# Kernel optimization log

Hardware: AMD Instinct MI355X
Metric: run time of the kernel (lower is better)

Reference implementation:

```python
import jax, jax.numpy as jnp
import numpy as np
from jax import lax

NB_DIGITS = 2
BASE = 10
NUMS = BASE ** NB_DIGITS            # 100 possible values per number
SUMS = 2 * (NUMS - 1) + 1           # 199 possible sums (circuit roots)
B = 4096                            # logical batch size
N_IMAGES = B * 2 * NB_DIGITS        # 16384 digit images


def setup_inputs() -> dict:
    key = jax.random.key(0)
    ks = jax.random.split(key, 11)
    s = 0.1
    return {
        "images": jax.random.normal(ks[0], (N_IMAGES, 1, 28, 28), jnp.float32),
        "conv1_w": jax.random.normal(ks[1], (6, 1, 5, 5), jnp.float32) * s,
        "conv1_b": jax.random.normal(ks[2], (6,), jnp.float32) * s,
        "conv2_w": jax.random.normal(ks[3], (16, 6, 5, 5), jnp.float32) * s,
        "conv2_b": jax.random.normal(ks[4], (16,), jnp.float32) * s,
        "fc1_w": jax.random.normal(ks[5], (120, 256), jnp.float32) * s,
        "fc1_b": jax.random.normal(ks[6], (120,), jnp.float32) * s,
        "fc2_w": jax.random.normal(ks[7], (84, 120), jnp.float32) * s,
        "fc2_b": jax.random.normal(ks[8], (84,), jnp.float32) * s,
        "fc3_w": jax.random.normal(ks[9], (10, 84), jnp.float32) * s,
        "fc3_b": jax.random.normal(ks[10], (10,), jnp.float32) * s,
    }


def _conv(x, w, b):
    y = lax.conv_general_dilated(x, w, (1, 1), 'VALID',
                                 dimension_numbers=('NCHW', 'OIHW', 'NCHW'))
    return y + b[None, :, None, None]


def _maxpool2(x):
    return lax.reduce_window(x, -jnp.inf, lax.max, (1, 1, 2, 2), (1, 1, 2, 2), 'VALID')


def _lenet(x, c1w, c1b, c2w, c2b, f1w, f1b, f2w, f2b, f3w, f3b):
    x = jax.nn.relu(_maxpool2(_conv(x, c1w, c1b)))   # [N,6,12,12]
    x = jax.nn.relu(_maxpool2(_conv(x, c2w, c2b)))   # [N,16,4,4]
    x = x.reshape(-1, 16 * 4 * 4)
    x = jax.nn.relu(x @ f1w.T + f1b)
    x = jax.nn.relu(x @ f2w.T + f2b)
    x = x @ f3w.T + f3b
    return jax.nn.log_softmax(x, axis=-1)            # [N,10]


def _circuit(lp):
    # lp: [B, 2*NB_DIGITS, 10] per-digit log-probs.
    # Vars layout from get_circuit: positions 0..NB_DIGITS-1 = n1 digits (MSB first),
    # positions NB_DIGITS..2*NB_DIGITS-1 = n2 digits. Neg-literal weights are 0 in
    # log space (the `zeros` arg), so each model's weight = sum of digit log-probs;
    # OR over models = logsumexp grouped by n1+n2.
    d = jnp.arange(NUMS)
    hi, lo = d // BASE, d % BASE
    lp1 = lp[:, 0, hi] + lp[:, 1, lo]                # [B, NUMS] log P(n1=k)
    lp2 = lp[:, 2, hi] + lp[:, 3, lo]                # [B, NUMS] log P(n2=k)
    M = (lp1[:, :, None] + lp2[:, None, :]).reshape(lp.shape[0], -1)  # [B, NUMS^2]
    seg = (jnp.arange(NUMS)[:, None] + jnp.arange(NUMS)[None, :]).reshape(-1)
    Mf = M.T                                          # [NUMS^2, B]
    m = jax.ops.segment_max(Mf, seg, num_segments=SUMS)              # [SUMS, B]
    ssum = jax.ops.segment_sum(jnp.exp(Mf - m[seg]), seg, num_segments=SUMS)
    return (jnp.log(ssum) + m).T                      # [B, SUMS] log P(sum=s)


def reference(images, conv1_w, conv1_b, conv2_w, conv2_b,
              fc1_w, fc1_b, fc2_w, fc2_b, fc3_w, fc3_b):
    logp = _lenet(images, conv1_w, conv1_b, conv2_w, conv2_b,
                  fc1_w, fc1_b, fc2_w, fc2_b, fc3_w, fc3_b)   # [N_IMAGES,10]
    lp = logp.reshape(B, 2 * NB_DIGITS, BASE)
    return _circuit(lp)
```

## Files before the change

### kernel.cpp

```cpp
#include <hip/hip_runtime.h>
#include <hip/hip_bf16.h>
#include <math.h>

#define SUMS 199
#define NBLK 1024

typedef __attribute__((ext_vector_type(8))) short short8;
typedef __attribute__((ext_vector_type(4))) float float4v;

union Frag8 { short8 v; unsigned u[4]; uint4 q; };

static __device__ inline unsigned pk_bf16(float a, float b) {
    __hip_bfloat162 h = __float22bfloat162_rn(make_float2(a, b));
    union { __hip_bfloat162 h; unsigned u; } c; c.h = h; return c.u;
}

__global__ __launch_bounds__(256) void convert_weights(
    const float* __restrict__ f1w, const float* __restrict__ f2w,
    const float* __restrict__ f3w, const float* __restrict__ c1w,
    const float* __restrict__ c2w, uint4* __restrict__ ws)
{
    const int g = blockIdx.x * 256 + threadIdx.x;
    if (g >= 6400) return;
    float v[8];
    if (g < 5824) {
        const float* W; int O, K, ld, nt, s, l;
        if (g < 4096)      { W = f1w; O = 120; K = 256; ld = 256; nt = g >> 9; s = (g >> 6) & 7; l = g & 63; }
        else if (g < 5632) { const int f = g - 4096; W = f2w; O = 84; K = 120; ld = 120; nt = f >> 8; s = (f >> 6) & 3; l = f & 63; }
        else               { const int f = g - 5632; W = f3w; O = 10; K = 84;  ld = 84;  nt = 0; s = f >> 6; l = f & 63; }
        const int o = nt * 16 + (l & 15);
        #pragma unroll
        for (int j = 0; j < 8; ++j) {
            const int k = 32 * s + 8 * (l >> 4) + j;
            v[j] = (o < O && k < K) ? W[o * ld + k] : 0.f;
        }
    } else if (g < 6336) {
        const int f = g - 5824, s = f >> 6, l = f & 63;
        const int c = l & 15, h = l >> 4;
        const int pos = 4 * s + h;
        const int ky = pos / 5, kx = pos % 5;
        const bool ok = (pos < 25);
        #pragma unroll
        for (int jp = 0; jp < 4; ++jp) {
            v[2 * jp]     = (ok && 2 * jp < 6)     ? c2w[c * 150 + (2 * jp) * 25 + ky * 5 + kx]     : 0.f;
            v[2 * jp + 1] = (ok && 2 * jp + 1 < 6) ? c2w[c * 150 + (2 * jp + 1) * 25 + ky * 5 + kx] : 0.f;
        }
    } else {
        const int l = (g - 6336) & 63;
        const int c = l & 15, h = l >> 4;
        const int oc = c >> 1, xs = c & 1;
        #pragma unroll
        for (int j = 0; j < 8; ++j) {
            const int p = h * 4 + (j >> 1);
            float w = 0.f;
            if (p < 15 && c < 12) {
                const int ky = p / 3, kx = 2 * (p % 3) + (j & 1) - xs;
                if (kx >= 0 && kx < 5) w = c1w[oc * 25 + ky * 5 + kx];
            }
            v[j] = w;
        }
    }
    uint4 r;
    r.x = pk_bf16(v[0], v[1]); r.y = pk_bf16(v[2], v[3]);
    r.z = pk_bf16(v[4], v[5]); r.w = pk_bf16(v[6], v[7]);
    ws[g] = r;
}

__global__ __launch_bounds__(256, 4) void lenet_circuit_kernel(
    const float* __restrict__ images,
    const float* __restrict__ c1b, const float* __restrict__ c2b,
    const float* __restrict__ f1b, const float* __restrict__ f2b,
    const float* __restrict__ f3b, const uint4* __restrict__ wsb,
    float* __restrict__ out)
{
    __shared__ __align__(16) unsigned char s_mem[39680];
    unsigned*       imgu = (unsigned*)s_mem;
    uint2*          imgw = (uint2*)s_mem;
    unsigned short* p1s  = (unsigned short*)(s_mem + 12672);
    const uint4*    p1u4 = (const uint4*)(s_mem + 12672);
    unsigned*       A1d  = (unsigned*)(s_mem + 31232);
    const uint4*    A1q  = (const uint4*)(s_mem + 31232);
    float*          pgf  = (float*)(s_mem + 7680);
    float*          Hf   = (float*)(s_mem + 8448);
    float*          Lf   = (float*)(s_mem + 8768);

    const int t = threadIdx.x, bid = blockIdx.x;
    const int lane = t & 63, wav = t >> 6;
    const int c = lane & 15, h = lane >> 4;
    const uint4 z4 = {0u, 0u, 0u, 0u};

    {
        uint4* pz = (uint4*)(s_mem + 12672);
        for (int i = t; i < 1160; i += 256) pz[i] = z4;
    }
    Frag8 a1; a1.q = wsb[6336 + lane];
    Frag8 w2[7];
    #pragma unroll
    for (int s = 0; s < 7; ++s) w2[s].q = wsb[5824 + s * 64 + lane];
    int koff[7];
    #pragma unroll
    for (int s = 0; s < 7; ++s) {
        const int pos = 4 * s + h;
        koff[s] = (pos < 25) ? (pos / 5) * 12 + (pos % 5) : 0;
    }
    int pd[4];
    #pragma unroll
    for (int q = 0; q < 4; ++q) {
        const int p = 4 * h + q;
        pd[q] = (p < 15) ? (p / 3) * 14 + (p % 3) : 0;
    }
    float bias0 = 0.f, bias1 = 0.f;
    if (h < 3) { bias0 = c1b[2 * h]; bias1 = c1b[2 * h + 1]; }
    const float b2v = c2b[c];

    float4 pf[7];
    {
        const float4* g1 = (const float4*)(images + (size_t)bid * 12544 + 6272);
        #pragma unroll
        for (int k = 0; k < 6; ++k) pf[k] = g1[t + 256 * k];
        if (t < 32) pf[6] = g1[1536 + t];
    }

    auto do_conv1 = [&]() {
        const int n = c, img = n >> 1;
        const int imb = img * 396 + (n & 1) * 14;
        for (int qy = wav * 3; qy < wav * 3 + 3; ++qy) {
            #pragma unroll
            for (int qx = 0; qx < 12; ++qx) {
                const int base = imb + qy * 28 + qx;
                Frag8 bf;
                #pragma unroll
                for (int q = 0; q < 4; ++q) bf.u[q] = imgu[base + pd[q]];
                float4v acc = {0.f, 0.f, 0.f, 0.f};
                acc = __builtin_amdgcn_mfma_f32_16x16x32_bf16(a1.v, bf.v, acc, 0, 0, 0);
                float v0 = fmaxf(acc[0], acc[1]);
                float v1 = fmaxf(acc[2], acc[3]);
                v0 = fmaxf(v0, __shfl_xor(v0, 1));
                v1 = fmaxf(v1, __shfl_xor(v1, 1));
                if ((n & 1) == 0 && h < 3) {
                    const unsigned pkv = pk_bf16(fmaxf(v0 + bias0, 0.f),
                                                 fmaxf(v1 + bias1, 0.f));
                    *(unsigned*)&p1s[img * 1160 + qy * 96 + qx * 8 + 2 * h] = pkv;
                }
            }
        }
    };
    auto do_conv2 = [&](int pass) {
        const int pxl = (c & 1) + 2 * ((c >> 2) & 1);
        const int pyl = ((c >> 1) & 1) + 2 * ((c >> 3) & 1);
        #pragma unroll
        for (int ii = 0; ii < 2; ++ii) {
            const int i0 = 2 * wav + ii;
            #pragma unroll
            for (int mt = 0; mt < 4; ++mt) {
                const int px = pxl + 4 * (mt & 1), py = pyl + 4 * (mt >> 1);
                const int base = i0 * 145 + py * 12 + px;
                float4v acc = {0.f, 0.f, 0.f, 0.f};
                #pragma unroll
                for (int s = 0; s < 7; ++s) {
                    Frag8 af; af.q = p1u4[base + koff[s]];
                    acc = __builtin_amdgcn_mfma_f32_16x16x32_bf16(af.v, w2[s].v, acc, 0, 0, 0);
                }
                const float p = fmaxf(fmaxf(acc[0], acc[1]), fmaxf(acc[2], acc[3]));
                float v = fmaxf(p + b2v, 0.f);
                const float vp = __shfl_xor(v, 16);
                if ((h & 1) == 0) {
                    const int qy = (h >> 1) + 2 * (mt >> 1);
                    A1d[(pass * 8 + i0) * 132 + c * 8 + qy * 2 + (mt & 1)] = pk_bf16(v, vp);
                }
            }
        }
    };

    {
        const float4* g = (const float4*)(images + (size_t)bid * 12544);
        for (int i = t; i < 1568; i += 256) {
            const float4 v = g[i];
            const int im = i / 196, j = i % 196;
            uint2 w; w.x = pk_bf16(v.x, v.y); w.y = pk_bf16(v.z, v.w);
            imgw[im * 198 + j] = w;
        }
    }
    __syncthreads();
    do_conv1();
    __syncthreads();
    do_conv2(0);
    {
        #pragma unroll
        for (int k = 0; k < 6; ++k) {
            const int i = t + 256 * k;
            const int im = i / 196, j = i % 196;
            uint2 w; w.x = pk_bf16(pf[k].x, pf[k].y); w.y = pk_bf16(pf[k].z, pf[k].w);
            imgw[im * 198 + j] = w;
        }
        if (t < 32) {
            const int i = 1536 + t;
            const int im = i / 196, j = i % 196;
            uint2 w; w.x = pk_bf16(pf[6].x, pf[6].y); w.y = pk_bf16(pf[6].z, pf[6].w);
            imgw[im * 198 + j] = w;
        }
    }
    __syncthreads();
    do_conv1();
    __syncthreads();
    do_conv2(1);
    __syncthreads();

    {
        unsigned* A2d = (unsigned*)s_mem;
        if (t < 64) A2d[(t >> 2) * 68 + 60 + (t & 3)] = 0u;
        float4v acc0 = {0.f, 0.f, 0.f, 0.f}, acc1 = acc0;
        const int nt0 = 2 * wav;
        #pragma unroll
        for (int s = 0; s < 8; ++s) {
            Frag8 af; af.q = A1q[c * 33 + 4 * s + h];
            Frag8 b0; b0.q = wsb[(nt0 * 8 + s) * 64 + lane];
            Frag8 b1; b1.q = wsb[((nt0 + 1) * 8 + s) * 64 + lane];
            acc0 = __builtin_amdgcn_mfma_f32_16x16x32_bf16(af.v, b0.v, acc0, 0, 0, 0);
            acc1 = __builtin_amdgcn_mfma_f32_16x16x32_bf16(af.v, b1.v, acc1, 0, 0, 0);
        }
        #pragma unroll
        for (int ntl = 0; ntl < 2; ++ntl) {
            const int o = 32 * wav + 16 * ntl + c;
            const float bias = (o < 120) ? f1b[o] : 0.f;
            #pragma unroll
            for (int r = 0; r < 4; ++r) {
                float v = fmaxf((ntl ? acc1[r] : acc0[r]) + bias, 0.f);
                const float vp = __shfl_xor(v, 1);
                if ((c & 1) == 0 && o < 120)
                    A2d[(4 * h + r) * 68 + (o >> 1)] = pk_bf16(v, vp);
            }
        }
    }
    __syncthreads();

    {
        unsigned* A3d = (unsigned*)(s_mem + 4352);
        if (t < 96) A3d[(t / 6) * 52 + 42 + (t % 6)] = 0u;
        if (wav < 3) {
            const uint4* A2q = (const uint4*)s_mem;
            float4v acc0 = {0.f, 0.f, 0.f, 0.f}, acc1 = acc0;
            const int nt0 = 2 * wav;
            #pragma unroll
            for (int s = 0; s < 4; ++s) {
                Frag8 af; af.q = A2q[c * 17 + 4 * s + h];
                Frag8 b0; b0.q = wsb[4096 + (nt0 * 4 + s) * 64 + lane];
                Frag8 b1; b1.q = wsb[4096 + ((nt0 + 1) * 4 + s) * 64 + lane];
                acc0 = __builtin_amdgcn_mfma_f32_16x16x32_bf16(af.v, b0.v, acc0, 0, 0, 0);
                acc1 = __builtin_amdgcn_mfma_f32_16x16x32_bf16(af.v, b1.v, acc1, 0, 0, 0);
            }
            #pragma unroll
            for (int ntl = 0; ntl < 2; ++ntl) {
                const int o = 32 * wav + 16 * ntl + c;
                const float bias = (o < 84) ? f2b[o] : 0.f;
                #pragma unroll
                for (int r = 0; r < 4; ++r) {
                    float v = fmaxf((ntl ? acc1[r] : acc0[r]) + bias, 0.f);
                    const float vp = __shfl_xor(v, 1);
                    if ((c & 1) == 0 && o < 84)
                        A3d[(4 * h + r) * 52 + (o >> 1)] = pk_bf16(v, vp);
                }
            }
        }
    }
    __syncthreads();

    {
        const uint4* A3q = (const uint4*)(s_mem + 4352);
        float4v acc = {0.f, 0.f, 0.f, 0.f};
        #pragma unroll
        for (int s = 0; s < 3; ++s) {
            Frag8 af; af.q = A3q[c * 13 + 4 * s + h];
            Frag8 b; b.q = wsb[5632 + s * 64 + lane];
            acc = __builtin_amdgcn_mfma_f32_16x16x32_bf16(af.v, b.v, acc, 0, 0, 0);
        }
        const float bias = (c < 10) ? f3b[c] : 0.f;
        float x[4], m[4], e[4], sm[4];
        #pragma unroll
        for (int r = 0; r < 4; ++r) {
            x[r] = (c < 10) ? (acc[r] + bias) : -INFINITY;
            m[r] = x[r];
        }
        #pragma unroll
        for (int d = 1; d <= 8; d <<= 1)
            #pragma unroll
            for (int r = 0; r < 4; ++r) m[r] = fmaxf(m[r], __shfl_xor(m[r], d));
        #pragma unroll
        for (int r = 0; r < 4; ++r) { e[r] = (c < 10) ? expf(x[r] - m[r]) : 0.f; sm[r] = e[r]; }
        #pragma unroll
        for (int d = 1; d <= 8; d <<= 1)
            #pragma unroll
            for (int r = 0; r < 4; ++r) sm[r] += __shfl_xor(sm[r], d);
        if (c < 10 && h == wav) {
            #pragma unroll
            for (int r = 0; r < 4; ++r)
                pgf[(4 * wav + r) * 12 + c] = e[r] / sm[r];
        }

        if (lane < 38) {
            const int isH = (lane < 19), b = isH ? lane : lane - 19;
            const float* pg = pgf + 4 * wav * 12;
            const float* PA = pg + (isH ? 0 : 12);
            const float* PB = pg + (isH ? 24 : 36);
            const int ilo = (b > 9) ? b - 9 : 0;
            const int ihi = (b < 9) ? b : 9;
            float s = 0.f;
            for (int i = ilo; i <= ihi; ++i) s += PA[i] * PB[b - i];
            (isH ? Hf : Lf)[wav * 20 + b] = s;
        }

        const float* H = Hf + wav * 20;
        const float* L = Lf + wav * 20;
        for (int s = lane; s < SUMS; s += 64) {
            const int bmin = (s > 18) ? (s - 9) / 10 : 0;
            int bmax = s / 10; if (bmax > 18) bmax = 18;
            float sum = 0.f;
            for (int b = bmin; b <= bmax; ++b) sum += H[b] * L[s - 10 * b];
            out[((size_t)bid * 4 + wav) * SUMS + s] = logf(sum);
        }
    }
}

extern "C" void kernel_launch(void* const* d_in, const int* in_sizes, int n_in,
                              void* d_out, int out_size, void* d_ws, size_t ws_size,
                              hipStream_t stream) {
    const float* images = (const float*)d_in[0];
    const float* c1w = (const float*)d_in[1];
    const float* c1b = (const float*)d_in[2];
    const float* c2w = (const float*)d_in[3];
    const float* c2b = (const float*)d_in[4];
    const float* f1w = (const float*)d_in[5];
    const float* f1b = (const float*)d_in[6];
    const float* f2w = (const float*)d_in[7];
    const float* f2b = (const float*)d_in[8];
    const float* f3w = (const float*)d_in[9];
    const float* f3b = (const float*)d_in[10];
    float* out = (float*)d_out;

    convert_weights<<<25, 256, 0, stream>>>(f1w, f2w, f3w, c1w, c2w, (uint4*)d_ws);
    lenet_circuit_kernel<<<NBLK, 256, 0, stream>>>(
        images, c1b, c2b, f1b, f2b, f3b, (const uint4*)d_ws, out);
}
```

Baseline: 135.7 us.

## Make each wave own two images through conv stages to drop block barriers

Re-partitions the image staging, conv1 and the LDS zeroing so that each wave handles exactly the two images it later consumes in conv2. The intent is to turn block-wide __syncthreads between the staging, conv1 and conv2 phases into intra-wave dependencies and remove four barriers. The conv1 lane mapping changes (qx groups per lane, shuffle by 2). Correctness now depends on wave-lockstep ordering of LDS writes and reads within a wave, with no explicit wave-level fence, and the second staging pass overwrites the image buffer right after conv1 in the same wave.

```diff
diff --git a/kernel.cpp b/kernel.cpp
--- a/kernel.cpp
+++ b/kernel.cpp
@@ -89,9 +89,11 @@
     const int c = lane & 15, h = lane >> 4;
     const uint4 z4 = {0u, 0u, 0u, 0u};
 
-    {
-        uint4* pz = (uint4*)(s_mem + 12672);
-        for (int i = t; i < 1160; i += 256) pz[i] = z4;
+    const int qxo = c >> 2, parity = (c >> 1) & 1, irel = c & 1;
+
+    {
+        uint4* pz = (uint4*)(s_mem + 12672) + 2 * wav * 145;
+        for (int j = lane; j < 290; j += 64) pz[j] = z4;
     }
     Frag8 a1; a1.q = wsb[6336 + lane];
     Frag8 w2[7];
@@ -115,19 +117,33 @@
 
     float4 pf[7];
     {
-        const float4* g1 = (const float4*)(images + (size_t)bid * 12544 + 6272);
-        #pragma unroll
-        for (int k = 0; k < 6; ++k) pf[k] = g1[t + 256 * k];
-        if (t < 32) pf[6] = g1[1536 + t];
-    }
-
+        const float4* g1 = (const float4*)(images + (size_t)bid * 12544 + 6272) + 392 * wav;
+        #pragma unroll
+        for (int k = 0; k < 7; ++k) {
+            const int i = lane + 64 * k;
+            if (i < 392) pf[k] = g1[i];
+        }
+    }
+
+    auto do_stage1 = [&]() {
+        #pragma unroll
+        for (int k = 0; k < 7; ++k) {
+            const int i = lane + 64 * k;
+            if (i < 392) {
+                const int im = 2 * wav + (i >= 196);
+                const int j = i - ((i >= 196) ? 196 : 0);
+                uint2 wv; wv.x = pk_bf16(pf[k].x, pf[k].y); wv.y = pk_bf16(pf[k].z, pf[k].w);
+                imgw[im * 198 + j] = wv;
+            }
+        }
+    };
     auto do_conv1 = [&]() {
-        const int n = c, img = n >> 1;
-        const int imb = img * 396 + (n & 1) * 14;
-        for (int qy = wav * 3; qy < wav * 3 + 3; ++qy) {
-            #pragma unroll
-            for (int qx = 0; qx < 12; ++qx) {
-                const int base = imb + qy * 28 + qx;
+        const int img = 2 * wav + irel;
+        const int imb = img * 396 + parity * 14 + qxo;
+        for (int qy = 0; qy < 12; ++qy) {
+            #pragma unroll
+            for (int qxg = 0; qxg < 3; ++qxg) {
+                const int base = imb + qy * 28 + qxg * 4;
                 Frag8 bf;
                 #pragma unroll
                 for (int q = 0; q < 4; ++q) bf.u[q] = imgu[base + pd[q]];
@@ -135,12 +151,12 @@
                 acc = __builtin_amdgcn_mfma_f32_16x16x32_bf16(a1.v, bf.v, acc, 0, 0, 0);
                 float v0 = fmaxf(acc[0], acc[1]);
                 float v1 = fmaxf(acc[2], acc[3]);
-                v0 = fmaxf(v0, __shfl_xor(v0, 1));
-                v1 = fmaxf(v1, __shfl_xor(v1, 1));
-                if ((n & 1) == 0 && h < 3) {
-                    const unsigned pkv = pk_bf16(fmaxf(v0 + bias0, 0.f),
-                                                 fmaxf(v1 + bias1, 0.f));
-                    *(unsigned*)&p1s[img * 1160 + qy * 96 + qx * 8 + 2 * h] = pkv;
+                v0 = fmaxf(v0, __shfl_xor(v0, 2));
+                v1 = fmaxf(v1, __shfl_xor(v1, 2));
+                if (parity == 0 && h < 3) {
+                    const int qx = qxg * 4 + qxo;
+                    *(unsigned*)&p1s[img * 1160 + qy * 96 + qx * 8 + 2 * h] =
+                        pk_bf16(fmaxf(v0 + bias0, 0.f), fmaxf(v1 + bias1, 0.f));
                 }
             }
         }
@@ -173,36 +189,23 @@
     };
 
     {
-        const float4* g = (const float4*)(images + (size_t)bid * 12544);
-        for (int i = t; i < 1568; i += 256) {
-            const float4 v = g[i];
-            const int im = i / 196, j = i % 196;
-            uint2 w; w.x = pk_bf16(v.x, v.y); w.y = pk_bf16(v.z, v.w);
-            imgw[im * 198 + j] = w;
-        }
-    }
-    __syncthreads();
+        const float4* g = (const float4*)(images + (size_t)bid * 12544) + 392 * wav;
+        #pragma unroll
+        for (int k = 0; k < 7; ++k) {
+            const int i = lane + 64 * k;
+            if (i < 392) {
+                const float4 v = g[i];
+                const int im = 2 * wav + (i >= 196);
+                const int j = i - ((i >= 196) ? 196 : 0);
+                uint2 wv; wv.x = pk_bf16(v.x, v.y); wv.y = pk_bf16(v.z, v.w);
+                imgw[im * 198 + j] = wv;
+            }
+        }
+    }
     do_conv1();
-    __syncthreads();
+    do_stage1();
     do_conv2(0);
-    {
-        #pragma unroll
-        for (int k = 0; k < 6; ++k) {
-            const int i = t + 256 * k;
-            const int im = i / 196, j = i % 196;
-            uint2 w; w.x = pk_bf16(pf[k].x, pf[k].y); w.y = pk_bf16(pf[k].z, pf[k].w);
-            imgw[im * 198 + j] = w;
-        }
-        if (t < 32) {
-            const int i = 1536 + t;
-            const int im = i / 196, j = i % 196;
-            uint2 w; w.x = pk_bf16(pf[6].x, pf[6].y); w.y = pk_bf16(pf[6].z, pf[6].w);
-            imgw[im * 198 + j] = w;
-        }
-    }
-    __syncthreads();
     do_conv1();
-    __syncthreads();
     do_conv2(1);
     __syncthreads();
 
```

New measurement: 136.0 us. Within noise of the previous version (+0.2%).
